# Kernel tuning notes

Hardware: AMD Instinct MI355X
Metric: run time of the kernel (lower is better)

Reference implementation:

```python
import jax, jax.numpy as jnp
import numpy as np

VOL_SIZE = 1.0  # config.render.volume_size


def _make_grid(G, vol_size):
    # pytorch3d Volumes.get_coord_grid(world_coordinates=True): axis-aligned grid
    # centered at origin, spacing = voxel_size = vol_size/G, last dim is (x,y,z)
    # with x varying along W, y along H, z along D.
    m = (G - 1) / 2.0 * (vol_size / G)
    lin = jnp.linspace(-m, m, G, dtype=jnp.float32)
    zz, yy, xx = jnp.meshgrid(lin, lin, lin, indexing='ij')
    return jnp.stack([xx, yy, zz], axis=-1)  # [G,G,G,3]


def _grid_sample_3d(vol, grid):
    # vol: [N,C,D,H,W]; grid: [N,Dg,Hg,Wg,3] xyz in [-1,1].
    # Matches torch F.grid_sample(mode='bilinear', padding_mode='zeros', align_corners=False).
    N, C, D, H, W = vol.shape
    ix = ((grid[..., 0] + 1.0) * W - 1.0) * 0.5
    iy = ((grid[..., 1] + 1.0) * H - 1.0) * 0.5
    iz = ((grid[..., 2] + 1.0) * D - 1.0) * 0.5
    x0f, y0f, z0f = jnp.floor(ix), jnp.floor(iy), jnp.floor(iz)
    tx, ty, tz = ix - x0f, iy - y0f, iz - z0f
    x0, y0, z0 = x0f.astype(jnp.int32), y0f.astype(jnp.int32), z0f.astype(jnp.int32)

    def per_batch(v, z0, y0, x0, tx, ty, tz):
        # v: [C,D,H,W]; index/weight maps: [Dg,Hg,Wg]
        def corner(z, y, x):
            valid = (z >= 0) & (z < D) & (y >= 0) & (y < H) & (x >= 0) & (x < W)
            zc = jnp.clip(z, 0, D - 1)
            yc = jnp.clip(y, 0, H - 1)
            xc = jnp.clip(x, 0, W - 1)
            return v[:, zc, yc, xc] * valid[None]  # [C,Dg,Hg,Wg]
        z1, y1, x1 = z0 + 1, y0 + 1, x0 + 1
        acc = jnp.zeros((C,) + z0.shape, dtype=v.dtype)
        for zc, wz in ((z0, 1.0 - tz), (z1, tz)):
            for yc, wy in ((y0, 1.0 - ty), (y1, ty)):
                for xc, wx in ((x0, 1.0 - tx), (x1, tx)):
                    acc = acc + corner(zc, yc, xc) * (wz * wy * wx)[None]
        return acc

    return jax.vmap(per_batch)(vol, z0, y0, x0, tx, ty, tz)


def reference(voxels, camPoses_cv2, grid_size):
    B, t, C, D, H, W = voxels.shape
    G = grid_size
    m = (G - 1) / 2.0 * (VOL_SIZE / G)  # grid_coord_max
    grid_coord = _make_grid(G, VOL_SIZE)  # [G,G,G,3]

    # T = pose_0 @ pose_1^{-1}, per (B, t-1) pair
    pose0 = jnp.broadcast_to(camPoses_cv2[:, 0:1], (B, t - 1, 4, 4)).reshape(B * (t - 1), 4, 4)
    pose1 = camPoses_cv2[:, 1:].reshape(B * (t - 1), 4, 4)
    T = pose0 @ jnp.linalg.inv(pose1)

    # homogeneous transform of world grid points: cam = R @ p + trans
    pts = grid_coord.reshape(-1, 3)  # [N=G^3, 3]
    R, trans = T[:, :3, :3], T[:, :3, 3]
    cam = jnp.einsum('nij,pj->npi', R, pts) + trans[:, None, :]  # [B*(t-1), N, 3]
    sample_grid = (cam / m).reshape(B * (t - 1), D, H, W, 3)

    warped = _grid_sample_3d(voxels[:, 1:].reshape(B * (t - 1), C, D, H, W), sample_grid)
    out = jnp.concatenate([voxels[:, 0:1], warped.reshape(B, t - 1, C, D, H, W)], axis=1)
    return out


def setup_inputs() -> dict:
    key = jax.random.key(0)
    kv, ka, kt = jax.random.split(key, 3)
    B, t, C, G = 2, 5, 16, 64
    voxels = jax.random.normal(kv, (B, t, C, G, G, G), dtype=jnp.float32)
    # build valid SE(3)-ish camera poses (orthonormal rotation + small translation)
    A = jax.random.normal(ka, (B, t, 3, 3), dtype=jnp.float32)
    Q, _ = jnp.linalg.qr(A)
    det = jnp.linalg.det(Q)
    Q = Q * jnp.sign(det)[..., None, None]  # ensure det=+1
    trans = 0.2 * jax.random.normal(kt, (B, t, 3), dtype=jnp.float32)
    top = jnp.concatenate([Q, trans[..., None]], axis=-1)  # [B,t,3,4]
    bottom = jnp.broadcast_to(jnp.array([0.0, 0.0, 0.0, 1.0], jnp.float32), (B, t, 1, 4))
    camPoses_cv2 = jnp.concatenate([top, bottom], axis=-2)  # [B,t,4,4]
    return {"voxels": voxels, "camPoses_cv2": camPoses_cv2, "grid_size": G}
```

## Files before the change

### kernel.cpp

```cpp
#include <hip/hip_runtime.h>

#define G3_    (64 * 64 * 64)
#define CCH    16
#define BB     2
#define TT     5
#define NPOSE  8
#define LSTRIDE 17

__global__ void pose_kernel(const float* __restrict__ cam, float* __restrict__ T)
{
    int n = threadIdx.x;
    if (n >= NPOSE) return;
    int b = n / (TT - 1);
    int j = n % (TT - 1);
    const float* p0 = cam + (size_t)(b * TT + 0) * 16;
    const float* p1 = cam + (size_t)(b * TT + j + 1) * 16;

    float R0[3][3], t0[3], R1[3][3], t1[3];
    #pragma unroll
    for (int r = 0; r < 3; ++r) {
        #pragma unroll
        for (int c = 0; c < 3; ++c) { R0[r][c] = p0[r * 4 + c]; R1[r][c] = p1[r * 4 + c]; }
        t0[r] = p0[r * 4 + 3];
        t1[r] = p1[r * 4 + 3];
    }
    float R[3][3], tr[3];
    #pragma unroll
    for (int r = 0; r < 3; ++r)
        #pragma unroll
        for (int c = 0; c < 3; ++c)
            R[r][c] = R0[r][0] * R1[c][0] + R0[r][1] * R1[c][1] + R0[r][2] * R1[c][2];
    #pragma unroll
    for (int r = 0; r < 3; ++r)
        tr[r] = t0[r] - (R[r][0] * t1[0] + R[r][1] * t1[1] + R[r][2] * t1[2]);

    float* o = T + n * 12;
    #pragma unroll
    for (int r = 0; r < 3; ++r) {
        #pragma unroll
        for (int c = 0; c < 3; ++c) o[r * 3 + c] = R[r][c];
        o[9 + r] = tr[r];
    }
}

__global__ __launch_bounds__(256) void copy0_kernel(const float* __restrict__ vox,
                                                    float* __restrict__ out)
{
    int tid = blockIdx.x * 256 + threadIdx.x;
    int b = tid >> 20;
    int r = tid & ((1 << 20) - 1);
    size_t base = (size_t)(b * TT) * CCH * G3_;
    const float4* s = (const float4*)(vox + base);
    float4* d = (float4*)(out + base);
    d[r] = s[r];
}

__global__ __launch_bounds__(256) void warp_kernel(const float* __restrict__ vox,
                                                   const float* __restrict__ T,
                                                   float* __restrict__ out)
{
    __shared__ float lds[4096];
    const int tid = threadIdx.x;
    const int bid = blockIdx.x;
    const int n   = bid >> 9;
    const int t6  = bid & 511;
    const int ox  = (t6 & 7) << 3;
    const int oy  = ((t6 >> 3) & 7) << 3;
    const int oz  = (t6 >> 6) << 3;
    const int b   = n >> 2, j = n & 3;

    #pragma unroll
    for (int i = 0; i < 16; ++i) lds[tid + i * 256] = 0.0f;

    const float* Tn = T + n * 12;
    float R00 = Tn[0], R01 = Tn[1], R02 = Tn[2];
    float R10 = Tn[3], R11 = Tn[4], R12 = Tn[5];
    float R20 = Tn[6], R21 = Tn[7], R22 = Tn[8];
    float trx = Tn[9], try_ = Tn[10], trz = Tn[11];

    const float S  = 1.0f / 64.0f;
    const float SC = 32.0f / 0.4921875f;
    const float ax = SC * R00 * S, bx = SC * R01 * S, cx = SC * R02 * S;
    const float ay = SC * R10 * S, by = SC * R11 * S, cy = SC * R12 * S;
    const float az = SC * R20 * S, bz = SC * R21 * S, cz = SC * R22 * S;
    const float kx = -31.5f * (ax + bx + cx) + SC * trx + 31.5f;
    const float ky = -31.5f * (ay + by + cy) + SC * try_ + 31.5f;
    const float kz = -31.5f * (az + bz + cz) + SC * trz + 31.5f;

    float x0a = ax * ox, x0b = ax * (ox + 7);
    float x1a = bx * oy, x1b = bx * (oy + 7);
    float x2a = cx * oz, x2b = cx * (oz + 7);
    float min_ix = kx + fminf(x0a, x0b) + fminf(x1a, x1b) + fminf(x2a, x2b);
    float max_ix = kx + fmaxf(x0a, x0b) + fmaxf(x1a, x1b) + fmaxf(x2a, x2b);
    float y0a = ay * ox, y0b = ay * (ox + 7);
    float y1a = by * oy, y1b = by * (oy + 7);
    float y2a = cy * oz, y2b = cy * (oz + 7);
    float min_iy = ky + fminf(y0a, y0b) + fminf(y1a, y1b) + fminf(y2a, y2b);
    float max_iy = ky + fmaxf(y0a, y0b) + fmaxf(y1a, y1b) + fmaxf(y2a, y2b);
    float z0a = az * ox, z0b = az * (ox + 7);
    float z1a = bz * oy, z1b = bz * (oy + 7);
    float z2a = cz * oz, z2b = cz * (oz + 7);
    float min_iz = kz + fminf(z0a, z0b) + fminf(z1a, z1b) + fminf(z2a, z2b);
    float max_iz = kz + fmaxf(z0a, z0b) + fmaxf(z1a, z1b) + fmaxf(z2a, z2b);

    int xlo = min(max((int)floorf(min_ix), 0), 63);
    int xhi = min(max((int)floorf(max_ix) + 1, 0), 63);
    int ylo = min(max((int)floorf(min_iy), 0), 63);
    int yhi = min(max((int)floorf(max_iy) + 1, 0), 63);
    int zlo = min(max((int)floorf(min_iz), 0), 63);
    int zhi = min(max((int)floorf(max_iz) + 1, 0), 63);
    int sx = xhi - xlo + 1;
    int sy = yhi - ylo + 1;
    int sz = zhi - zlo + 1;
    const int lstep = sy * LSTRIDE;

    float w[2][6];
    int   ia[2][4], rxa[2][2], soff[2];
    #pragma unroll
    for (int k = 0; k < 2; ++k) {
        int o  = tid + (k << 8);
        int gx = ox + (o & 7);
        int gy = oy + ((o >> 3) & 7);
        int gz = oz + (o >> 6);
        float ix = kx + ax * gx + bx * gy + cx * gz;
        float iy = ky + ay * gx + by * gy + cy * gz;
        float iz = kz + az * gx + bz * gy + cz * gz;
        float fx = floorf(ix), fy = floorf(iy), fz = floorf(iz);
        float tx = ix - fx, ty = iy - fy, tz = iz - fz;
        int X0 = (int)fx, Y0 = (int)fy, Z0 = (int)fz;
        w[k][0] = ((unsigned)X0 < 64u) ? (1.0f - tx) : 0.0f;
        w[k][1] = ((unsigned)(X0 + 1) < 64u) ? tx : 0.0f;
        w[k][2] = ((unsigned)Y0 < 64u) ? (1.0f - ty) : 0.0f;
        w[k][3] = ((unsigned)(Y0 + 1) < 64u) ? ty : 0.0f;
        w[k][4] = ((unsigned)Z0 < 64u) ? (1.0f - tz) : 0.0f;
        w[k][5] = ((unsigned)(Z0 + 1) < 64u) ? tz : 0.0f;
        int rx0 = min(max(X0     - xlo, 0), sx - 1);
        int rx1 = min(max(X0 + 1 - xlo, 0), sx - 1);
        int ry0 = min(max(Y0     - ylo, 0), sy - 1) * LSTRIDE;
        int ry1 = min(max(Y0 + 1 - ylo, 0), sy - 1) * LSTRIDE;
        int rz0 = min(max(Z0     - zlo, 0), sz - 1) * lstep;
        int rz1 = min(max(Z0 + 1 - zlo, 0), sz - 1) * lstep;
        ia[k][0] = rz0 + ry0;
        ia[k][1] = rz0 + ry1;
        ia[k][2] = rz1 + ry0;
        ia[k][3] = rz1 + ry1;
        rxa[k][0] = rx0;
        rxa[k][1] = rx1;
        soff[k] = (gz << 12) + (gy << 6) + gx;
    }

    const size_t fb = (size_t)((b * TT + j + 1) * CCH) * G3_;
    const float* vbase = vox + fb;
    float* obase = out + fb;

    const int lane16 = tid & 15;
    const int row16  = tid >> 4;
    const bool act   = (lane16 < sx) && (row16 < sy);
    const int grow   = (zlo << 12) + ((ylo + row16) << 6) + xlo + lane16;
    const int lrow   = row16 * LSTRIDE + lane16;

    for (int c = 0; c < CCH; ++c) {
        __syncthreads();
        if (act) {
            const float* gp = vbase + (size_t)c * G3_ + grow;
            int la = lrow;
            for (int zz = 0; zz < sz; ++zz) {
                lds[la] = *gp;
                gp += 4096;
                la += lstep;
            }
        }
        __syncthreads();
        float* op = obase + (size_t)c * G3_;
        #pragma unroll
        for (int k = 0; k < 2; ++k) {
            int r0 = rxa[k][0], r1 = rxa[k][1];
            float v000 = lds[ia[k][0] + r0], v001 = lds[ia[k][0] + r1];
            float v010 = lds[ia[k][1] + r0], v011 = lds[ia[k][1] + r1];
            float v100 = lds[ia[k][2] + r0], v101 = lds[ia[k][2] + r1];
            float v110 = lds[ia[k][3] + r0], v111 = lds[ia[k][3] + r1];
            float t00 = v000 * w[k][0] + v001 * w[k][1];
            float t01 = v010 * w[k][0] + v011 * w[k][1];
            float t10 = v100 * w[k][0] + v101 * w[k][1];
            float t11 = v110 * w[k][0] + v111 * w[k][1];
            float u0  = t00 * w[k][2] + t01 * w[k][3];
            float u1  = t10 * w[k][2] + t11 * w[k][3];
            op[soff[k]] = u0 * w[k][4] + u1 * w[k][5];
        }
    }
}

extern "C" void kernel_launch(void* const* d_in, const int* in_sizes, int n_in,
                              void* d_out, int out_size, void* d_ws, size_t ws_size,
                              hipStream_t stream)
{
    const float* vox = (const float*)d_in[0];
    const float* cam = (const float*)d_in[1];
    float* out = (float*)d_out;
    float* Tws = (float*)d_ws;

    hipLaunchKernelGGL(pose_kernel, dim3(1), dim3(64), 0, stream, cam, Tws);
    hipLaunchKernelGGL(copy0_kernel, dim3(8192), dim3(256), 0, stream, vox, out);
    hipLaunchKernelGGL(warp_kernel, dim3(4096), dim3(256), 0, stream, vox, Tws, out);
}
```

Measured before the change: 413.2 us.

## Double-buffer LDS tiles and prefetch next channel into registers

Splits shared memory into two buffers and, while the current channel is interpolated, loads the next channel's slab into registers and then writes it to the alternate buffer. This hides global load latency behind compute and cuts the barriers per channel from two to one. In exchange it doubles LDS use, which may lower occupancy, adds up to 15 staging registers, and assumes the z extent never exceeds MAXZ. It also includes a redundant rewrite of the z-bound computation.

```diff
diff --git a/kernel.cpp b/kernel.cpp
--- a/kernel.cpp
+++ b/kernel.cpp
@@ -2,10 +2,11 @@
 
 #define G3_    (64 * 64 * 64)
 #define CCH    16
-#define BB     2
 #define TT     5
 #define NPOSE  8
 #define LSTRIDE 17
+#define MAXZ   15
+#define BUF    4096
 
 __global__ void pose_kernel(const float* __restrict__ cam, float* __restrict__ T)
 {
@@ -59,7 +60,7 @@
                                                    const float* __restrict__ T,
                                                    float* __restrict__ out)
 {
-    __shared__ float lds[4096];
+    __shared__ float lds[2 * BUF];
     const int tid = threadIdx.x;
     const int bid = blockIdx.x;
     const int n   = bid >> 9;
@@ -70,7 +71,7 @@
     const int b   = n >> 2, j = n & 3;
 
     #pragma unroll
-    for (int i = 0; i < 16; ++i) lds[tid + i * 256] = 0.0f;
+    for (int i = 0; i < 32; ++i) lds[tid + i * 256] = 0.0f;
 
     const float* Tn = T + n * 12;
     float R00 = Tn[0], R01 = Tn[1], R02 = Tn[2];
@@ -98,10 +99,11 @@
     float min_iy = ky + fminf(y0a, y0b) + fminf(y1a, y1b) + fminf(y2a, y2b);
     float max_iy = ky + fmaxf(y0a, y0b) + fmaxf(y1a, y1b) + fmaxf(y2a, y2b);
     float z0a = az * ox, z0b = az * (ox + 7);
-    float z1a = bz * oy, z1b = bz * (oy + 7);
+    float z1a = bz * oy, z1b = bz * (ox ? oz : oz);
+    z1b = bz * (oy + 7);
     float z2a = cz * oz, z2b = cz * (oz + 7);
-    float min_iz = kz + fminf(z0a, z0b) + fminf(z1a, z1b) + fminf(z2a, z2b);
-    float max_iz = kz + fmaxf(z0a, z0b) + fmaxf(z1a, z1b) + fmaxf(z2a, z2b);
+    float min_iz = kz + fminf(z0a, z0b) + fminf(bz * oy, z1b) + fminf(z2a, z2b);
+    float max_iz = kz + fmaxf(z0a, z0b) + fmaxf(bz * oy, z1b) + fmaxf(z2a, z2b);
 
     int xlo = min(max((int)floorf(min_ix), 0), 63);
     int xhi = min(max((int)floorf(max_ix) + 1, 0), 63);
@@ -159,26 +161,36 @@
     const int grow   = (zlo << 12) + ((ylo + row16) << 6) + xlo + lane16;
     const int lrow   = row16 * LSTRIDE + lane16;
 
+    if (act) {
+        const float* gp = vbase + grow;
+        int la = lrow;
+        for (int zz = 0; zz < sz; ++zz) {
+            lds[la] = gp[(size_t)zz << 12];
+            la += lstep;
+        }
+    }
+    __syncthreads();
+
     for (int c = 0; c < CCH; ++c) {
-        __syncthreads();
-        if (act) {
-            const float* gp = vbase + (size_t)c * G3_ + grow;
-            int la = lrow;
-            for (int zz = 0; zz < sz; ++zz) {
-                lds[la] = *gp;
-                gp += 4096;
-                la += lstep;
+        float stg[MAXZ];
+        const bool pre = (c + 1 < CCH);
+        if (pre && act) {
+            const float* gp = vbase + (size_t)(c + 1) * G3_ + grow;
+            #pragma unroll
+            for (int zz = 0; zz < MAXZ; ++zz) {
+                if (zz < sz) stg[zz] = gp[(size_t)zz << 12];
             }
         }
-        __syncthreads();
+
+        const float* buf = lds + (c & 1) * BUF;
         float* op = obase + (size_t)c * G3_;
         #pragma unroll
         for (int k = 0; k < 2; ++k) {
             int r0 = rxa[k][0], r1 = rxa[k][1];
-            float v000 = lds[ia[k][0] + r0], v001 = lds[ia[k][0] + r1];
-            float v010 = lds[ia[k][1] + r0], v011 = lds[ia[k][1] + r1];
-            float v100 = lds[ia[k][2] + r0], v101 = lds[ia[k][2] + r1];
-            float v110 = lds[ia[k][3] + r0], v111 = lds[ia[k][3] + r1];
+            float v000 = buf[ia[k][0] + r0], v001 = buf[ia[k][0] + r1];
+            float v010 = buf[ia[k][1] + r0], v011 = buf[ia[k][1] + r1];
+            float v100 = buf[ia[k][2] + r0], v101 = buf[ia[k][2] + r1];
+            float v110 = buf[ia[k][3] + r0], v111 = buf[ia[k][3] + r1];
             float t00 = v000 * w[k][0] + v001 * w[k][1];
             float t01 = v010 * w[k][0] + v011 * w[k][1];
             float t10 = v100 * w[k][0] + v101 * w[k][1];
@@ -187,6 +199,15 @@
             float u1  = t10 * w[k][2] + t11 * w[k][3];
             op[soff[k]] = u0 * w[k][4] + u1 * w[k][5];
         }
+
+        if (pre && act) {
+            float* wbuf = lds + ((c + 1) & 1) * BUF;
+            #pragma unroll
+            for (int zz = 0; zz < MAXZ; ++zz) {
+                if (zz < sz) wbuf[lrow + zz * lstep] = stg[zz];
+            }
+        }
+        __syncthreads();
     }
 }
 
```

Result: faster. 380.9 us (-7.8%).
